# Kernel tuning notes

Hardware: AMD Instinct MI355X
Metric: run time of the kernel (lower is better)

The kernel has to match this reference:

```python
import jax, jax.numpy as jnp
import numpy as np

B, CIN, C, H, W = 8, 256, 128, 128, 128
BN_EPS = 1e-5
EPS = 1e-12


def _bn_params(k, c):
    k1, k2, k3, k4 = jax.random.split(k, 4)
    gamma = jax.random.uniform(k1, (c,), minval=0.5, maxval=1.5)
    beta = jax.random.normal(k2, (c,)) * 0.1
    mean = jax.random.normal(k3, (c,)) * 0.1
    var = jax.random.uniform(k4, (c,), minval=0.5, maxval=1.5)
    return gamma, beta, mean, var


def _xavier(k, cout, cin):
    lim = np.sqrt(6.0 / (cin + cout))
    return jax.random.uniform(k, (cout, cin), minval=-lim, maxval=lim)


def setup_inputs() -> dict:
    key = jax.random.key(0)
    ks = jax.random.split(key, 16)
    inp = {
        'target_task_feats': jax.random.normal(ks[0], (B, CIN, H, W), dtype=jnp.float32),
        'source_task_feats': jax.random.normal(ks[1], (B, CIN, H, W), dtype=jnp.float32),
        'q_w1': _xavier(ks[2], C, CIN), 'q_w2': _xavier(ks[3], C, C),
        'k_w1': _xavier(ks[4], C, CIN), 'k_w2': _xavier(ks[5], C, C),
        'v_w': _xavier(ks[6], C, CIN),
    }
    for name, kk, c in [('q1', ks[7], C), ('q2', ks[8], C), ('k1', ks[9], C), ('k2', ks[10], C), ('v', ks[11], C)]:
        g, b, m, v = _bn_params(kk, c)
        inp[f'{name}_g'], inp[f'{name}_b'], inp[f'{name}_m'], inp[f'{name}_v'] = g, b, m, v
    return inp


def _conv_bn(x, w, g, b, m, v):
    # 1x1 conv (no bias) + eval-mode BatchNorm, fused scale/shift
    y = jnp.einsum('bchw,oc->bohw', x, w)
    scale = (g / jnp.sqrt(v + BN_EPS))[None, :, None, None]
    shift = (b - m * g / jnp.sqrt(v + BN_EPS))[None, :, None, None]
    return y * scale + shift


def reference(target_task_feats, source_task_feats,
              q_w1, q_w2, k_w1, k_w2, v_w,
              q1_g, q1_b, q1_m, q1_v,
              q2_g, q2_b, q2_m, q2_v,
              k1_g, k1_b, k1_m, k1_v,
              k2_g, k2_b, k2_m, k2_v,
              v_g, v_b, v_m, v_v):
    b = target_task_feats.shape[0]
    # key / value from source
    k_h = jax.nn.relu(_conv_bn(source_task_feats, k_w1, k1_g, k1_b, k1_m, k1_v))
    key = jax.nn.softplus(_conv_bn(k_h, k_w2, k2_g, k2_b, k2_m, k2_v)).reshape(b, C, -1)  # [B,C,Ns]
    value = jax.nn.relu(_conv_bn(source_task_feats, v_w, v_g, v_b, v_m, v_v)).reshape(b, C, -1)  # [B,C,Ns]
    # query from target
    q_h = jax.nn.relu(_conv_bn(target_task_feats, q_w1, q1_g, q1_b, q1_m, q1_v))
    query = jax.nn.softplus(_conv_bn(q_h, q_w2, q2_g, q2_b, q2_m, q2_v)).reshape(b, C, -1)  # [B,C,Nt]
    # linear attention: KV^T then Q
    S = jnp.einsum('bcn,bdn->bcd', value, key)      # [B,C,C]
    Z = key.sum(axis=2)                              # [B,C]
    denom = jnp.einsum('bc,bcn->bn', Z, query)[:, None, :]  # [B,1,Nt]
    out = jnp.einsum('bcd,bdn->bcn', S, query) / jnp.maximum(denom, EPS)
    return out.reshape(b, C, H, W)
```

## Files before the change

### kernel.cpp

```cpp
#include <hip/hip_runtime.h>
#include <math.h>

typedef __attribute__((ext_vector_type(8))) short bf8v;
typedef __attribute__((ext_vector_type(4))) float f4v;

#define B_      8
#define CIN_    256
#define C_      128
#define NPIX_   16384
#define EPS_    1e-12f
#define BN_EPS_ 1e-5f

#define OFF_WK1  0u
#define OFF_WV   65536u
#define OFF_WQ1  131072u
#define OFF_WK2  196608u
#define OFF_WQ2  229376u
#define OFF_BIAS 262144u
#define OFF_S    264704u
#define OFF_Z    788992u
#define OFF_SBF  793088u
#define OFF_VAL  1055232u
#define OFF_KEY  34609664u

__device__ __forceinline__ unsigned short f2bf(float f) {
    unsigned u = __float_as_uint(f);
    unsigned r = u + 0x7fffu + ((u >> 16) & 1u);
    return (unsigned short)(r >> 16);
}
__device__ __forceinline__ float lo16(unsigned v){ return __uint_as_float(v << 16); }
__device__ __forceinline__ float hi16(unsigned v){ return __uint_as_float(v & 0xffff0000u); }
__device__ __forceinline__ float softplus_f(float x) {
    return fmaxf(x, 0.f) + __logf(1.f + __expf(-fabsf(x)));
}
__device__ __forceinline__ f4v MFMA(bf8v a, bf8v b, f4v c) {
    return __builtin_amdgcn_mfma_f32_16x16x32_bf16(a, b, c, 0, 0, 0);
}

struct PrepPtrs {
    const float* w[5];
    const float* g[5];
    const float* be[5];
    const float* mu[5];
    const float* va[5];
    unsigned short* wout[5];
    float* bout[5];
};

__global__ void prep_kernel(PrepPtrs p) {
    int idx = blockIdx.x * 256 + threadIdx.x;
    if (idx < 131072) {
        int conv, local, sh;
        if (idx < 32768)       { conv = 0; local = idx;          sh = 8; }
        else if (idx < 65536)  { conv = 1; local = idx - 32768;  sh = 8; }
        else if (idx < 98304)  { conv = 2; local = idx - 65536;  sh = 8; }
        else if (idx < 114688) { conv = 3; local = idx - 98304;  sh = 7; }
        else                   { conv = 4; local = idx - 114688; sh = 7; }
        int o = local >> sh;
        float scale = p.g[conv][o] * rsqrtf(p.va[conv][o] + BN_EPS_);
        p.wout[conv][local] = f2bf(p.w[conv][local] * scale);
    } else if (idx < 131712) {
        int j = idx - 131072;
        int conv = j >> 7;
        int o = j & 127;
        float scale = p.g[conv][o] * rsqrtf(p.va[conv][o] + BN_EPS_);
        p.bout[conv][o] = p.be[conv][o] - p.mu[conv][o] * scale;
    }
}

__global__ __launch_bounds__(256)
void srcKV(const float* __restrict__ src,
           const unsigned short* __restrict__ Wk1, const unsigned short* __restrict__ Wv,
           const unsigned short* __restrict__ Wk2, const float* __restrict__ bias,
           unsigned short* __restrict__ valg, unsigned short* __restrict__ keyg)
{
    __shared__ __align__(16) char smem[52224];
    unsigned short* xT = (unsigned short*)smem;
    unsigned short* hT = (unsigned short*)(smem + 33792);

    const int tid = threadIdx.x;
    const int L = tid & 63, w = tid >> 6;
    const int lr = L & 15, qd = L >> 4;
    const int b = blockIdx.y;
    const int gn0 = blockIdx.x * 64;
    const int m0 = w * 32;
    const int kbq = qd * 8;
    const float* bk1 = bias + 0;
    const float* bvp = bias + 128;
    const float* bk2 = bias + 384;

    #pragma unroll
    for (int s = 0; s < 4; s++) {
        int id = tid + s * 256;
        int n4 = (id & 15) * 4;
        int k0 = (id >> 4) * 4;
        float4 r[4];
        #pragma unroll
        for (int i = 0; i < 4; i++)
            r[i] = *(const float4*)(src + (size_t)(b * 256 + k0 + i) * NPIX_ + gn0 + n4);
        #pragma unroll
        for (int j = 0; j < 4; j++) {
            ushort4 t;
            t.x = f2bf(((const float*)&r[0])[j]);
            t.y = f2bf(((const float*)&r[1])[j]);
            t.z = f2bf(((const float*)&r[2])[j]);
            t.w = f2bf(((const float*)&r[3])[j]);
            *(ushort4*)(xT + (n4 + j) * 264 + k0) = t;
        }
    }
    __syncthreads();

    f4v zz = {0.f, 0.f, 0.f, 0.f};
    f4v hAcc[2][4], vAcc[2][4];
    #pragma unroll
    for (int mt = 0; mt < 2; mt++)
        #pragma unroll
        for (int nt = 0; nt < 4; nt++) { hAcc[mt][nt] = zz; vAcc[mt][nt] = zz; }
    #pragma unroll
    for (int ks = 0; ks < 8; ks++) {
        const int kb = ks * 32 + kbq;
        bf8v a1[2], a2[2], bx[4];
        #pragma unroll
        for (int mt = 0; mt < 2; mt++) {
            a1[mt] = *(const bf8v*)(Wk1 + (m0 + mt * 16 + lr) * 256 + kb);
            a2[mt] = *(const bf8v*)(Wv  + (m0 + mt * 16 + lr) * 256 + kb);
        }
        #pragma unroll
        for (int nt = 0; nt < 4; nt++)
            bx[nt] = *(const bf8v*)(xT + (nt * 16 + lr) * 264 + kb);
        #pragma unroll
        for (int mt = 0; mt < 2; mt++)
            #pragma unroll
            for (int nt = 0; nt < 4; nt++) {
                hAcc[mt][nt] = MFMA(a1[mt], bx[nt], hAcc[mt][nt]);
                vAcc[mt][nt] = MFMA(a2[mt], bx[nt], vAcc[mt][nt]);
            }
    }
    #pragma unroll
    for (int mt = 0; mt < 2; mt++) {
        const float4 b4 = *(const float4*)(bk1 + m0 + mt * 16 + qd * 4);
        #pragma unroll
        for (int nt = 0; nt < 4; nt++) {
            ushort4 t;
            t.x = f2bf(fmaxf(hAcc[mt][nt][0] + b4.x, 0.f));
            t.y = f2bf(fmaxf(hAcc[mt][nt][1] + b4.y, 0.f));
            t.z = f2bf(fmaxf(hAcc[mt][nt][2] + b4.z, 0.f));
            t.w = f2bf(fmaxf(hAcc[mt][nt][3] + b4.w, 0.f));
            *(ushort4*)(hT + (nt * 16 + lr) * 136 + m0 + mt * 16 + qd * 4) = t;
        }
    }
    __syncthreads();
    #pragma unroll
    for (int mt = 0; mt < 2; mt++) {
        const float4 b4 = *(const float4*)(bvp + m0 + mt * 16 + qd * 4);
        const float* bp = (const float*)&b4;
        #pragma unroll
        for (int nt = 0; nt < 4; nt++)
            #pragma unroll
            for (int r = 0; r < 4; r++)
                vAcc[mt][nt][r] = fmaxf(vAcc[mt][nt][r] + bp[r], 0.f);
    }

    f4v kAcc[2][4];
    #pragma unroll
    for (int mt = 0; mt < 2; mt++)
        #pragma unroll
        for (int nt = 0; nt < 4; nt++) kAcc[mt][nt] = zz;
    #pragma unroll
    for (int ks = 0; ks < 4; ks++) {
        const int kb = ks * 32 + kbq;
        bf8v a[2], bh[4];
        #pragma unroll
        for (int mt = 0; mt < 2; mt++)
            a[mt] = *(const bf8v*)(Wk2 + (m0 + mt * 16 + lr) * 128 + kb);
        #pragma unroll
        for (int nt = 0; nt < 4; nt++)
            bh[nt] = *(const bf8v*)(hT + (nt * 16 + lr) * 136 + kb);
        #pragma unroll
        for (int mt = 0; mt < 2; mt++)
            #pragma unroll
            for (int nt = 0; nt < 4; nt++)
                kAcc[mt][nt] = MFMA(a[mt], bh[nt], kAcc[mt][nt]);
    }
    __syncthreads();

    unsigned short* stgV = xT;
    unsigned short* stgK = hT;
    #pragma unroll
    for (int mt = 0; mt < 2; mt++) {
        const float4 b4 = *(const float4*)(bk2 + m0 + mt * 16 + qd * 4);
        const float* bp = (const float*)&b4;
        #pragma unroll
        for (int nt = 0; nt < 4; nt++)
            #pragma unroll
            for (int r = 0; r < 4; r++) {
                int m = m0 + mt * 16 + qd * 4 + r;
                stgV[m * 72 + nt * 16 + lr] = f2bf(vAcc[mt][nt][r]);
                stgK[m * 72 + nt * 16 + lr] = f2bf(softplus_f(kAcc[mt][nt][r] + bp[r]));
            }
    }
    __syncthreads();
    #pragma unroll
    for (int s = 0; s < 8; s++) {
        int id = tid + s * 256;
        int arr = id >> 10, rem = id & 1023;
        int c = rem >> 3, o = rem & 7;
        const unsigned short* sp = (arr ? stgK : stgV) + c * 72 + o * 8;
        uint4 d = *(const uint4*)sp;
        unsigned short* gp = (arr ? keyg : valg) + (size_t)(b * 128 + c) * NPIX_ + gn0 + o * 8;
        *(uint4*)gp = d;
    }
}

__global__ __launch_bounds__(256)
void skern(const unsigned short* __restrict__ valg, const unsigned short* __restrict__ keyg,
           float* __restrict__ Sbuf, float* __restrict__ Zbuf)
{
    __shared__ __align__(16) unsigned short vs[128 * 72];
    __shared__ __align__(16) unsigned short ks_[128 * 72];
    const int tid = threadIdx.x;
    const int L = tid & 63, w = tid >> 6;
    const int lr = L & 15, qd = L >> 4;
    const int b = blockIdx.x >> 5, ch = blockIdx.x & 31;
    const size_t nbase = (size_t)ch * 512;
    const int m0 = (w & 1) * 64, n0 = (w >> 1) * 64;

    f4v zz = {0.f, 0.f, 0.f, 0.f};
    f4v acc[4][4];
    #pragma unroll
    for (int mt = 0; mt < 4; mt++)
        #pragma unroll
        for (int nt = 0; nt < 4; nt++) acc[mt][nt] = zz;
    float zacc = 0.f;
    const int zc = tid >> 1, zh = tid & 1;

    for (int wd = 0; wd < 8; wd++) {
        const size_t nw = nbase + wd * 64;
        #pragma unroll
        for (int s = 0; s < 8; s++) {
            int id = tid + s * 256;
            int arr = id >> 10, rem = id & 1023;
            int c = rem >> 3, o = rem & 7;
            const unsigned short* g = (arr ? keyg : valg) + (size_t)(b * 128 + c) * NPIX_ + nw + o * 8;
            uint4 d = *(const uint4*)g;
            *(uint4*)((arr ? ks_ : vs) + c * 72 + o * 8) = d;
        }
        __syncthreads();
        #pragma unroll
        for (int kk = 0; kk < 2; kk++) {
            const int kb = kk * 32 + qd * 8;
            bf8v a[4], bb[4];
            #pragma unroll
            for (int mt = 0; mt < 4; mt++)
                a[mt] = *(const bf8v*)(vs + (m0 + mt * 16 + lr) * 72 + kb);
            #pragma unroll
            for (int nt = 0; nt < 4; nt++)
                bb[nt] = *(const bf8v*)(ks_ + (n0 + nt * 16 + lr) * 72 + kb);
            #pragma unroll
            for (int mt = 0; mt < 4; mt++)
                #pragma unroll
                for (int nt = 0; nt < 4; nt++)
                    acc[mt][nt] = MFMA(a[mt], bb[nt], acc[mt][nt]);
        }
        {
            const unsigned short* kr = ks_ + zc * 72 + zh * 32;
            #pragma unroll
            for (int p = 0; p < 4; p++) {
                uint4 t = *(const uint4*)(kr + p * 8);
                zacc += lo16(t.x) + hi16(t.x) + lo16(t.y) + hi16(t.y)
                      + lo16(t.z) + hi16(t.z) + lo16(t.w) + hi16(t.w);
            }
        }
        __syncthreads();
    }
    #pragma unroll
    for (int mt = 0; mt < 4; mt++)
        #pragma unroll
        for (int nt = 0; nt < 4; nt++)
            #pragma unroll
            for (int r = 0; r < 4; r++) {
                int m = m0 + mt * 16 + qd * 4 + r;
                int cN = n0 + nt * 16 + lr;
                atomicAdd(Sbuf + ((size_t)b * 128 + m) * 128 + cN, acc[mt][nt][r]);
            }
    atomicAdd(Zbuf + b * 128 + zc, zacc);
}

__global__ void cvts(const float* __restrict__ Sbuf, unsigned short* __restrict__ Sbf) {
    int i = blockIdx.x * 256 + threadIdx.x;
    if (i < 131072) Sbf[i] = f2bf(Sbuf[i]);
}

__global__ __launch_bounds__(256)
void tgtAttn(const float* __restrict__ tgt,
             const unsigned short* __restrict__ Wq1, const unsigned short* __restrict__ Wq2,
             const float* __restrict__ bias, const unsigned short* __restrict__ Sbf,
             const float* __restrict__ Zbuf, float* __restrict__ out)
{
    __shared__ __align__(16) char smem[51968];
    unsigned short* xT = (unsigned short*)smem;
    unsigned short* qT = (unsigned short*)(smem + 33792);
    float* dn  = (float*)(smem + 33792 + 17408);
    float* Zsh = dn + 64;

    const int tid = threadIdx.x;
    const int L = tid & 63, w = tid >> 6;
    const int lr = L & 15, qd = L >> 4;
    const int b = blockIdx.y;
    const int gn0 = blockIdx.x * 64;
    const int m0 = w * 32;
    const int kbq = qd * 8;
    const float* bq1 = bias + 256;
    const float* bq2 = bias + 512;

    if (tid < 128) Zsh[tid] = Zbuf[b * 128 + tid];
    #pragma unroll
    for (int s = 0; s < 4; s++) {
        int id = tid + s * 256;
        int n4 = (id & 15) * 4;
        int k0 = (id >> 4) * 4;
        float4 r[4];
        #pragma unroll
        for (int i = 0; i < 4; i++)
            r[i] = *(const float4*)(tgt + (size_t)(b * 256 + k0 + i) * NPIX_ + gn0 + n4);
        #pragma unroll
        for (int j = 0; j < 4; j++) {
            ushort4 t;
            t.x = f2bf(((const float*)&r[0])[j]);
            t.y = f2bf(((const float*)&r[1])[j]);
            t.z = f2bf(((const float*)&r[2])[j]);
            t.w = f2bf(((const float*)&r[3])[j]);
            *(ushort4*)(xT + (n4 + j) * 264 + k0) = t;
        }
    }
    __syncthreads();

    f4v zz = {0.f, 0.f, 0.f, 0.f};
    f4v acc1[2][4];
    #pragma unroll
    for (int mt = 0; mt < 2; mt++)
        #pragma unroll
        for (int nt = 0; nt < 4; nt++) acc1[mt][nt] = zz;
    #pragma unroll
    for (int ks = 0; ks < 8; ks++) {
        const int kb = ks * 32 + kbq;
        bf8v a[2], bx[4];
        #pragma unroll
        for (int mt = 0; mt < 2; mt++)
            a[mt] = *(const bf8v*)(Wq1 + (m0 + mt * 16 + lr) * 256 + kb);
        #pragma unroll
        for (int nt = 0; nt < 4; nt++)
            bx[nt] = *(const bf8v*)(xT + (nt * 16 + lr) * 264 + kb);
        #pragma unroll
        for (int mt = 0; mt < 2; mt++)
            #pragma unroll
            for (int nt = 0; nt < 4; nt++)
                acc1[mt][nt] = MFMA(a[mt], bx[nt], acc1[mt][nt]);
    }
    #pragma unroll
    for (int mt = 0; mt < 2; mt++) {
        const float4 b4 = *(const float4*)(bq1 + m0 + mt * 16 + qd * 4);
        #pragma unroll
        for (int nt = 0; nt < 4; nt++) {
            ushort4 t;
            t.x = f2bf(fmaxf(acc1[mt][nt][0] + b4.x, 0.f));
            t.y = f2bf(fmaxf(acc1[mt][nt][1] + b4.y, 0.f));
            t.z = f2bf(fmaxf(acc1[mt][nt][2] + b4.z, 0.f));
            t.w = f2bf(fmaxf(acc1[mt][nt][3] + b4.w, 0.f));
            *(ushort4*)(qT + (nt * 16 + lr) * 136 + m0 + mt * 16 + qd * 4) = t;
        }
    }
    __syncthreads();

    f4v acc2[2][4];
    #pragma unroll
    for (int mt = 0; mt < 2; mt++)
        #pragma unroll
        for (int nt = 0; nt < 4; nt++) acc2[mt][nt] = zz;
    #pragma unroll
    for (int ks = 0; ks < 4; ks++) {
        const int kb = ks * 32 + kbq;
        bf8v a[2], bh[4];
        #pragma unroll
        for (int mt = 0; mt < 2; mt++)
            a[mt] = *(const bf8v*)(Wq2 + (m0 + mt * 16 + lr) * 128 + kb);
        #pragma unroll
        for (int nt = 0; nt < 4; nt++)
            bh[nt] = *(const bf8v*)(qT + (nt * 16 + lr) * 136 + kb);
        #pragma unroll
        for (int mt = 0; mt < 2; mt++)
            #pragma unroll
            for (int nt = 0; nt < 4; nt++)
                acc2[mt][nt] = MFMA(a[mt], bh[nt], acc2[mt][nt]);
    }
    __syncthreads();
    #pragma unroll
    for (int mt = 0; mt < 2; mt++) {
        const float4 b4 = *(const float4*)(bq2 + m0 + mt * 16 + qd * 4);
        const float* bp = (const float*)&b4;
        #pragma unroll
        for (int nt = 0; nt < 4; nt++) {
            ushort4 t;
            t.x = f2bf(softplus_f(acc2[mt][nt][0] + bp[0]));
            t.y = f2bf(softplus_f(acc2[mt][nt][1] + bp[1]));
            t.z = f2bf(softplus_f(acc2[mt][nt][2] + bp[2]));
            t.w = f2bf(softplus_f(acc2[mt][nt][3] + bp[3]));
            *(ushort4*)(qT + (nt * 16 + lr) * 136 + m0 + mt * 16 + qd * 4) = t;
        }
    }
    __syncthreads();

    if (tid < 64) {
        const unsigned short* qr = qT + tid * 136;
        float s = 0.f;
        #pragma unroll
        for (int d = 0; d < 128; d += 8) {
            uint4 t = *(const uint4*)(qr + d);
            s = fmaf(Zsh[d + 0], lo16(t.x), s);
            s = fmaf(Zsh[d + 1], hi16(t.x), s);
            s = fmaf(Zsh[d + 2], lo16(t.y), s);
            s = fmaf(Zsh[d + 3], hi16(t.y), s);
            s = fmaf(Zsh[d + 4], lo16(t.z), s);
            s = fmaf(Zsh[d + 5], hi16(t.z), s);
            s = fmaf(Zsh[d + 6], lo16(t.w), s);
            s = fmaf(Zsh[d + 7], hi16(t.w), s);
        }
        dn[tid] = fmaxf(s, EPS_);
    }

    f4v oacc[2][4];
    #pragma unroll
    for (int mt = 0; mt < 2; mt++)
        #pragma unroll
        for (int nt = 0; nt < 4; nt++) oacc[mt][nt] = zz;
    #pragma unroll
    for (int ks = 0; ks < 4; ks++) {
        const int kb = ks * 32 + kbq;
        bf8v a[2], bq[4];
        #pragma unroll
        for (int mt = 0; mt < 2; mt++)
            a[mt] = *(const bf8v*)(Sbf + (size_t)b * 16384 + (m0 + mt * 16 + lr) * 128 + kb);
        #pragma unroll
        for (int nt = 0; nt < 4; nt++)
            bq[nt] = *(const bf8v*)(qT + (nt * 16 + lr) * 136 + kb);
        #pragma unroll
        for (int mt = 0; mt < 2; mt++)
            #pragma unroll
            for (int nt = 0; nt < 4; nt++)
                oacc[mt][nt] = MFMA(a[mt], bq[nt], oacc[mt][nt]);
    }
    __syncthreads();

    float inv[4];
    #pragma unroll
    for (int nt = 0; nt < 4; nt++) inv[nt] = 1.f / dn[nt * 16 + lr];
    #pragma unroll
    for (int mt = 0; mt < 2; mt++)
        #pragma unroll
        for (int nt = 0; nt < 4; nt++)
            #pragma unroll
            for (int r = 0; r < 4; r++) {
                int m = m0 + mt * 16 + qd * 4 + r;
                out[(size_t)(b * 128 + m) * NPIX_ + gn0 + nt * 16 + lr] = oacc[mt][nt][r] * inv[nt];
            }
}

extern "C" void kernel_launch(void* const* d_in, const int* in_sizes, int n_in,
                              void* d_out, int out_size, void* d_ws, size_t ws_size,
                              hipStream_t stream)
{
    const float* tgt = (const float*)d_in[0];
    const float* src = (const float*)d_in[1];
    char* ws = (char*)d_ws;
    unsigned short* Wk1 = (unsigned short*)(ws + OFF_WK1);
    unsigned short* Wv  = (unsigned short*)(ws + OFF_WV);
    unsigned short* Wq1 = (unsigned short*)(ws + OFF_WQ1);
    unsigned short* Wk2 = (unsigned short*)(ws + OFF_WK2);
    unsigned short* Wq2 = (unsigned short*)(ws + OFF_WQ2);
    float* bias = (float*)(ws + OFF_BIAS);
    float* Sbuf = (float*)(ws + OFF_S);
    float* Zbuf = (float*)(ws + OFF_Z);
    unsigned short* Sbf = (unsigned short*)(ws + OFF_SBF);
    unsigned short* valg = (unsigned short*)(ws + OFF_VAL);
    unsigned short* keyg = (unsigned short*)(ws + OFF_KEY);

    PrepPtrs p;
    p.w[0] = (const float*)d_in[4];
    p.w[1] = (const float*)d_in[6];
    p.w[2] = (const float*)d_in[2];
    p.w[3] = (const float*)d_in[5];
    p.w[4] = (const float*)d_in[3];
    const int gbase[5] = {15, 23, 7, 19, 11};
    for (int c = 0; c < 5; c++) {
        p.g[c]  = (const float*)d_in[gbase[c]];
        p.be[c] = (const float*)d_in[gbase[c] + 1];
        p.mu[c] = (const float*)d_in[gbase[c] + 2];
        p.va[c] = (const float*)d_in[gbase[c] + 3];
    }
    p.wout[0] = Wk1; p.wout[1] = Wv; p.wout[2] = Wq1; p.wout[3] = Wk2; p.wout[4] = Wq2;
    p.bout[0] = bias; p.bout[1] = bias + 128; p.bout[2] = bias + 256;
    p.bout[3] = bias + 384; p.bout[4] = bias + 512;

    hipMemsetAsync(ws + OFF_S, 0, 524288 + 4096, stream);
    hipLaunchKernelGGL(prep_kernel, dim3(515), dim3(256), 0, stream, p);
    hipLaunchKernelGGL(srcKV, dim3(256, 8), dim3(256), 0, stream,
                       src, Wk1, Wv, Wk2, bias, valg, keyg);
    hipLaunchKernelGGL(skern, dim3(256), dim3(256), 0, stream, valg, keyg, Sbuf, Zbuf);
    hipLaunchKernelGGL(cvts, dim3(512), dim3(256), 0, stream, Sbuf, Sbf);
    hipLaunchKernelGGL(tgtAttn, dim3(256, 8), dim3(256), 0, stream,
                       tgt, Wq1, Wq2, bias, Sbf, Zbuf, (float*)d_out);
}
```

Baseline: 453.9 us.

## Fuse source key/value projection with KV reduction into one kernel

Merges srcKV and skern into a single kernel, srcS. Each block loops over four 64-pixel tiles, computes value and key in shared memory, and accumulates V·K^T and the key sums in registers before issuing atomics to S and Z. This removes the global round trip of the bf16 key and value tensors (about 64 MB written and read) and one kernel launch. In exchange the grid drops from 2048 to 512 blocks, the per-tile work is serialized with extra barriers, and register pressure rises under launch_bounds(256,2).

```diff
diff --git a/kernel.cpp b/kernel.cpp
--- a/kernel.cpp
+++ b/kernel.cpp
@@ -20,8 +20,6 @@
 #define OFF_S    264704u
 #define OFF_Z    788992u
 #define OFF_SBF  793088u
-#define OFF_VAL  1055232u
-#define OFF_KEY  34609664u
 
 __device__ __forceinline__ unsigned short f2bf(float f) {
     unsigned u = __float_as_uint(f);
@@ -68,202 +66,152 @@
     }
 }
 
-__global__ __launch_bounds__(256)
-void srcKV(const float* __restrict__ src,
-           const unsigned short* __restrict__ Wk1, const unsigned short* __restrict__ Wv,
-           const unsigned short* __restrict__ Wk2, const float* __restrict__ bias,
-           unsigned short* __restrict__ valg, unsigned short* __restrict__ keyg)
+__global__ __launch_bounds__(256, 2)
+void srcS(const float* __restrict__ src,
+          const unsigned short* __restrict__ Wk1, const unsigned short* __restrict__ Wv,
+          const unsigned short* __restrict__ Wk2, const float* __restrict__ bias,
+          float* __restrict__ Sbuf, float* __restrict__ Zbuf)
 {
     __shared__ __align__(16) char smem[52224];
     unsigned short* xT = (unsigned short*)smem;
     unsigned short* hT = (unsigned short*)(smem + 33792);
+    unsigned short* stgV = xT;
+    unsigned short* stgK = hT;
 
     const int tid = threadIdx.x;
     const int L = tid & 63, w = tid >> 6;
     const int lr = L & 15, qd = L >> 4;
     const int b = blockIdx.y;
-    const int gn0 = blockIdx.x * 64;
     const int m0 = w * 32;
     const int kbq = qd * 8;
+    const int m0s = (w & 1) * 64, n0s = (w >> 1) * 64;
     const float* bk1 = bias + 0;
     const float* bvp = bias + 128;
     const float* bk2 = bias + 384;
 
-    #pragma unroll
-    for (int s = 0; s < 4; s++) {
-        int id = tid + s * 256;
-        int n4 = (id & 15) * 4;
-        int k0 = (id >> 4) * 4;
-        float4 r[4];
-        #pragma unroll
-        for (int i = 0; i < 4; i++)
-            r[i] = *(const float4*)(src + (size_t)(b * 256 + k0 + i) * NPIX_ + gn0 + n4);
-        #pragma unroll
-        for (int j = 0; j < 4; j++) {
-            ushort4 t;
-            t.x = f2bf(((const float*)&r[0])[j]);
-            t.y = f2bf(((const float*)&r[1])[j]);
-            t.z = f2bf(((const float*)&r[2])[j]);
-            t.w = f2bf(((const float*)&r[3])[j]);
-            *(ushort4*)(xT + (n4 + j) * 264 + k0) = t;
-        }
-    }
-    __syncthreads();
-
     f4v zz = {0.f, 0.f, 0.f, 0.f};
-    f4v hAcc[2][4], vAcc[2][4];
-    #pragma unroll
-    for (int mt = 0; mt < 2; mt++)
-        #pragma unroll
-        for (int nt = 0; nt < 4; nt++) { hAcc[mt][nt] = zz; vAcc[mt][nt] = zz; }
-    #pragma unroll
-    for (int ks = 0; ks < 8; ks++) {
-        const int kb = ks * 32 + kbq;
-        bf8v a1[2], a2[2], bx[4];
-        #pragma unroll
-        for (int mt = 0; mt < 2; mt++) {
-            a1[mt] = *(const bf8v*)(Wk1 + (m0 + mt * 16 + lr) * 256 + kb);
-            a2[mt] = *(const bf8v*)(Wv  + (m0 + mt * 16 + lr) * 256 + kb);
-        }
-        #pragma unroll
-        for (int nt = 0; nt < 4; nt++)
-            bx[nt] = *(const bf8v*)(xT + (nt * 16 + lr) * 264 + kb);
-        #pragma unroll
-        for (int mt = 0; mt < 2; mt++)
-            #pragma unroll
-            for (int nt = 0; nt < 4; nt++) {
-                hAcc[mt][nt] = MFMA(a1[mt], bx[nt], hAcc[mt][nt]);
-                vAcc[mt][nt] = MFMA(a2[mt], bx[nt], vAcc[mt][nt]);
-            }
-    }
-    #pragma unroll
-    for (int mt = 0; mt < 2; mt++) {
-        const float4 b4 = *(const float4*)(bk1 + m0 + mt * 16 + qd * 4);
-        #pragma unroll
-        for (int nt = 0; nt < 4; nt++) {
-            ushort4 t;
-            t.x = f2bf(fmaxf(hAcc[mt][nt][0] + b4.x, 0.f));
-            t.y = f2bf(fmaxf(hAcc[mt][nt][1] + b4.y, 0.f));
-            t.z = f2bf(fmaxf(hAcc[mt][nt][2] + b4.z, 0.f));
-            t.w = f2bf(fmaxf(hAcc[mt][nt][3] + b4.w, 0.f));
-            *(ushort4*)(hT + (nt * 16 + lr) * 136 + m0 + mt * 16 + qd * 4) = t;
-        }
-    }
-    __syncthreads();
-    #pragma unroll
-    for (int mt = 0; mt < 2; mt++) {
-        const float4 b4 = *(const float4*)(bvp + m0 + mt * 16 + qd * 4);
-        const float* bp = (const float*)&b4;
-        #pragma unroll
-        for (int nt = 0; nt < 4; nt++)
-            #pragma unroll
-            for (int r = 0; r < 4; r++)
-                vAcc[mt][nt][r] = fmaxf(vAcc[mt][nt][r] + bp[r], 0.f);
-    }
-
-    f4v kAcc[2][4];
-    #pragma unroll
-    for (int mt = 0; mt < 2; mt++)
-        #pragma unroll
-        for (int nt = 0; nt < 4; nt++) kAcc[mt][nt] = zz;
-    #pragma unroll
-    for (int ks = 0; ks < 4; ks++) {
-        const int kb = ks * 32 + kbq;
-        bf8v a[2], bh[4];
-        #pragma unroll
-        for (int mt = 0; mt < 2; mt++)
-            a[mt] = *(const bf8v*)(Wk2 + (m0 + mt * 16 + lr) * 128 + kb);
-        #pragma unroll
-        for (int nt = 0; nt < 4; nt++)
-            bh[nt] = *(const bf8v*)(hT + (nt * 16 + lr) * 136 + kb);
-        #pragma unroll
-        for (int mt = 0; mt < 2; mt++)
-            #pragma unroll
-            for (int nt = 0; nt < 4; nt++)
-                kAcc[mt][nt] = MFMA(a[mt], bh[nt], kAcc[mt][nt]);
-    }
-    __syncthreads();
-
-    unsigned short* stgV = xT;
-    unsigned short* stgK = hT;
-    #pragma unroll
-    for (int mt = 0; mt < 2; mt++) {
-        const float4 b4 = *(const float4*)(bk2 + m0 + mt * 16 + qd * 4);
-        const float* bp = (const float*)&b4;
-        #pragma unroll
-        for (int nt = 0; nt < 4; nt++)
-            #pragma unroll
-            for (int r = 0; r < 4; r++) {
-                int m = m0 + mt * 16 + qd * 4 + r;
-                stgV[m * 72 + nt * 16 + lr] = f2bf(vAcc[mt][nt][r]);
-                stgK[m * 72 + nt * 16 + lr] = f2bf(softplus_f(kAcc[mt][nt][r] + bp[r]));
-            }
-    }
-    __syncthreads();
-    #pragma unroll
-    for (int s = 0; s < 8; s++) {
-        int id = tid + s * 256;
-        int arr = id >> 10, rem = id & 1023;
-        int c = rem >> 3, o = rem & 7;
-        const unsigned short* sp = (arr ? stgK : stgV) + c * 72 + o * 8;
-        uint4 d = *(const uint4*)sp;
-        unsigned short* gp = (arr ? keyg : valg) + (size_t)(b * 128 + c) * NPIX_ + gn0 + o * 8;
-        *(uint4*)gp = d;
-    }
-}
-
-__global__ __launch_bounds__(256)
-void skern(const unsigned short* __restrict__ valg, const unsigned short* __restrict__ keyg,
-           float* __restrict__ Sbuf, float* __restrict__ Zbuf)
-{
-    __shared__ __align__(16) unsigned short vs[128 * 72];
-    __shared__ __align__(16) unsigned short ks_[128 * 72];
-    const int tid = threadIdx.x;
-    const int L = tid & 63, w = tid >> 6;
-    const int lr = L & 15, qd = L >> 4;
-    const int b = blockIdx.x >> 5, ch = blockIdx.x & 31;
-    const size_t nbase = (size_t)ch * 512;
-    const int m0 = (w & 1) * 64, n0 = (w >> 1) * 64;
-
-    f4v zz = {0.f, 0.f, 0.f, 0.f};
-    f4v acc[4][4];
+    f4v sAcc[4][4];
     #pragma unroll
     for (int mt = 0; mt < 4; mt++)
         #pragma unroll
-        for (int nt = 0; nt < 4; nt++) acc[mt][nt] = zz;
+        for (int nt = 0; nt < 4; nt++) sAcc[mt][nt] = zz;
     float zacc = 0.f;
     const int zc = tid >> 1, zh = tid & 1;
 
-    for (int wd = 0; wd < 8; wd++) {
-        const size_t nw = nbase + wd * 64;
-        #pragma unroll
-        for (int s = 0; s < 8; s++) {
+    for (int wd = 0; wd < 4; wd++) {
+        const int gn0 = blockIdx.x * 256 + wd * 64;
+
+        #pragma unroll
+        for (int s = 0; s < 4; s++) {
             int id = tid + s * 256;
-            int arr = id >> 10, rem = id & 1023;
-            int c = rem >> 3, o = rem & 7;
-            const unsigned short* g = (arr ? keyg : valg) + (size_t)(b * 128 + c) * NPIX_ + nw + o * 8;
-            uint4 d = *(const uint4*)g;
-            *(uint4*)((arr ? ks_ : vs) + c * 72 + o * 8) = d;
+            int n4 = (id & 15) * 4;
+            int k0 = (id >> 4) * 4;
+            float4 r[4];
+            #pragma unroll
+            for (int i = 0; i < 4; i++)
+                r[i] = *(const float4*)(src + (size_t)(b * 256 + k0 + i) * NPIX_ + gn0 + n4);
+            #pragma unroll
+            for (int j = 0; j < 4; j++) {
+                ushort4 t;
+                t.x = f2bf(((const float*)&r[0])[j]);
+                t.y = f2bf(((const float*)&r[1])[j]);
+                t.z = f2bf(((const float*)&r[2])[j]);
+                t.w = f2bf(((const float*)&r[3])[j]);
+                *(ushort4*)(xT + (n4 + j) * 264 + k0) = t;
+            }
         }
         __syncthreads();
-        #pragma unroll
-        for (int kk = 0; kk < 2; kk++) {
-            const int kb = kk * 32 + qd * 8;
-            bf8v a[4], bb[4];
-            #pragma unroll
-            for (int mt = 0; mt < 4; mt++)
-                a[mt] = *(const bf8v*)(vs + (m0 + mt * 16 + lr) * 72 + kb);
-            #pragma unroll
-            for (int nt = 0; nt < 4; nt++)
-                bb[nt] = *(const bf8v*)(ks_ + (n0 + nt * 16 + lr) * 72 + kb);
-            #pragma unroll
-            for (int mt = 0; mt < 4; mt++)
+
+        f4v hAcc[2][4], vAcc[2][4];
+        #pragma unroll
+        for (int mt = 0; mt < 2; mt++)
+            #pragma unroll
+            for (int nt = 0; nt < 4; nt++) { hAcc[mt][nt] = zz; vAcc[mt][nt] = zz; }
+        #pragma unroll
+        for (int ks = 0; ks < 8; ks++) {
+            const int kb = ks * 32 + kbq;
+            bf8v a1[2], a2[2], bx[4];
+            #pragma unroll
+            for (int mt = 0; mt < 2; mt++) {
+                a1[mt] = *(const bf8v*)(Wk1 + (m0 + mt * 16 + lr) * 256 + kb);
+                a2[mt] = *(const bf8v*)(Wv  + (m0 + mt * 16 + lr) * 256 + kb);
+            }
+            #pragma unroll
+            for (int nt = 0; nt < 4; nt++)
+                bx[nt] = *(const bf8v*)(xT + (nt * 16 + lr) * 264 + kb);
+            #pragma unroll
+            for (int mt = 0; mt < 2; mt++)
+                #pragma unroll
+                for (int nt = 0; nt < 4; nt++) {
+                    hAcc[mt][nt] = MFMA(a1[mt], bx[nt], hAcc[mt][nt]);
+                    vAcc[mt][nt] = MFMA(a2[mt], bx[nt], vAcc[mt][nt]);
+                }
+        }
+        #pragma unroll
+        for (int mt = 0; mt < 2; mt++) {
+            const float4 b4 = *(const float4*)(bk1 + m0 + mt * 16 + qd * 4);
+            #pragma unroll
+            for (int nt = 0; nt < 4; nt++) {
+                ushort4 t;
+                t.x = f2bf(fmaxf(hAcc[mt][nt][0] + b4.x, 0.f));
+                t.y = f2bf(fmaxf(hAcc[mt][nt][1] + b4.y, 0.f));
+                t.z = f2bf(fmaxf(hAcc[mt][nt][2] + b4.z, 0.f));
+                t.w = f2bf(fmaxf(hAcc[mt][nt][3] + b4.w, 0.f));
+                *(ushort4*)(hT + (nt * 16 + lr) * 136 + m0 + mt * 16 + qd * 4) = t;
+            }
+        }
+        __syncthreads();
+        #pragma unroll
+        for (int mt = 0; mt < 2; mt++) {
+            const float4 b4 = *(const float4*)(bvp + m0 + mt * 16 + qd * 4);
+            const float* bp = (const float*)&b4;
+            #pragma unroll
+            for (int nt = 0; nt < 4; nt++)
+                #pragma unroll
+                for (int r = 0; r < 4; r++)
+                    vAcc[mt][nt][r] = fmaxf(vAcc[mt][nt][r] + bp[r], 0.f);
+        }
+
+        f4v kAcc[2][4];
+        #pragma unroll
+        for (int mt = 0; mt < 2; mt++)
+            #pragma unroll
+            for (int nt = 0; nt < 4; nt++) kAcc[mt][nt] = zz;
+        #pragma unroll
+        for (int ks = 0; ks < 4; ks++) {
+            const int kb = ks * 32 + kbq;
+            bf8v a[2], bh[4];
+            #pragma unroll
+            for (int mt = 0; mt < 2; mt++)
+                a[mt] = *(const bf8v*)(Wk2 + (m0 + mt * 16 + lr) * 128 + kb);
+            #pragma unroll
+            for (int nt = 0; nt < 4; nt++)
+                bh[nt] = *(const bf8v*)(hT + (nt * 16 + lr) * 136 + kb);
+            #pragma unroll
+            for (int mt = 0; mt < 2; mt++)
                 #pragma unroll
                 for (int nt = 0; nt < 4; nt++)
-                    acc[mt][nt] = MFMA(a[mt], bb[nt], acc[mt][nt]);
-        }
+                    kAcc[mt][nt] = MFMA(a[mt], bh[nt], kAcc[mt][nt]);
+        }
+        __syncthreads();
+
+        #pragma unroll
+        for (int mt = 0; mt < 2; mt++) {
+            const float4 b4 = *(const float4*)(bk2 + m0 + mt * 16 + qd * 4);
+            const float* bp = (const float*)&b4;
+            #pragma unroll
+            for (int nt = 0; nt < 4; nt++)
+                #pragma unroll
+                for (int r = 0; r < 4; r++) {
+                    int m = m0 + mt * 16 + qd * 4 + r;
+                    stgV[m * 72 + nt * 16 + lr] = f2bf(vAcc[mt][nt][r]);
+                    stgK[m * 72 + nt * 16 + lr] = f2bf(softplus_f(kAcc[mt][nt][r] + bp[r]));
+                }
+        }
+        __syncthreads();
+
         {
-            const unsigned short* kr = ks_ + zc * 72 + zh * 32;
+            const unsigned short* kr = stgK + zc * 72 + zh * 32;
             #pragma unroll
             for (int p = 0; p < 4; p++) {
                 uint4 t = *(const uint4*)(kr + p * 8);
@@ -271,17 +219,34 @@
                       + lo16(t.z) + hi16(t.z) + lo16(t.w) + hi16(t.w);
             }
         }
+        #pragma unroll
+        for (int kk = 0; kk < 2; kk++) {
+            const int kb = kk * 32 + kbq;
+            bf8v a[4], bb[4];
+            #pragma unroll
+            for (int mt = 0; mt < 4; mt++)
+                a[mt] = *(const bf8v*)(stgV + (m0s + mt * 16 + lr) * 72 + kb);
+            #pragma unroll
+            for (int nt = 0; nt < 4; nt++)
+                bb[nt] = *(const bf8v*)(stgK + (n0s + nt * 16 + lr) * 72 + kb);
+            #pragma unroll
+            for (int mt = 0; mt < 4; mt++)
+                #pragma unroll
+                for (int nt = 0; nt < 4; nt++)
+                    sAcc[mt][nt] = MFMA(a[mt], bb[nt], sAcc[mt][nt]);
+        }
         __syncthreads();
     }
+
     #pragma unroll
     for (int mt = 0; mt < 4; mt++)
         #pragma unroll
         for (int nt = 0; nt < 4; nt++)
             #pragma unroll
             for (int r = 0; r < 4; r++) {
-                int m = m0 + mt * 16 + qd * 4 + r;
-                int cN = n0 + nt * 16 + lr;
-                atomicAdd(Sbuf + ((size_t)b * 128 + m) * 128 + cN, acc[mt][nt][r]);
+                int m = m0s + mt * 16 + qd * 4 + r;
+                int cN = n0s + nt * 16 + lr;
+                atomicAdd(Sbuf + ((size_t)b * 128 + m) * 128 + cN, sAcc[mt][nt][r]);
             }
     atomicAdd(Zbuf + b * 128 + zc, zacc);
 }
@@ -481,8 +446,6 @@
     float* Sbuf = (float*)(ws + OFF_S);
     float* Zbuf = (float*)(ws + OFF_Z);
     unsigned short* Sbf = (unsigned short*)(ws + OFF_SBF);
-    unsigned short* valg = (unsigned short*)(ws + OFF_VAL);
-    unsigned short* keyg = (unsigned short*)(ws + OFF_KEY);
 
     PrepPtrs p;
     p.w[0] = (const float*)d_in[4];
@@ -503,9 +466,8 @@
 
     hipMemsetAsync(ws + OFF_S, 0, 524288 + 4096, stream);
     hipLaunchKernelGGL(prep_kernel, dim3(515), dim3(256), 0, stream, p);
-    hipLaunchKernelGGL(srcKV, dim3(256, 8), dim3(256), 0, stream,
-                       src, Wk1, Wv, Wk2, bias, valg, keyg);
-    hipLaunchKernelGGL(skern, dim3(256), dim3(256), 0, stream, valg, keyg, Sbuf, Zbuf);
+    hipLaunchKernelGGL(srcS, dim3(64, 8), dim3(256), 0, stream,
+                       src, Wk1, Wv, Wk2, bias, Sbuf, Zbuf);
     hipLaunchKernelGGL(cvts, dim3(512), dim3(256), 0, stream, Sbuf, Sbf);
     hipLaunchKernelGGL(tgtAttn, dim3(256, 8), dim3(256), 0, stream,
                        tgt, Wq1, Wq2, bias, Sbf, Zbuf, (float*)d_out);
```

New measurement: 483.6 us. +6.5%, slower.
